# Optimization experiments

Measured on AMD Instinct MI355X. Metric: run time of the kernel, lower is better.

The kernel has to match this reference:

```python
import jax, jax.numpy as jnp
import numpy as np

HEADS = 8
DK = 64   # key_size (defaults to size_per_head)
DV = 64   # size_per_head
RATE = 4
OUT = HEADS * DV  # 512


def extract_seq_patches(x, kernel, rate):
    # x: [b, L, d] -> [b, L, kernel, d]; strided local window gather
    b, L, d = x.shape
    k_size = kernel + (rate - 1) * (kernel - 1)
    p_right = (k_size - 1) // 2
    p_left = k_size - 1 - p_right
    xp = jnp.pad(x, ((0, 0), (p_left, p_right), (0, 0)))
    patches = [xp[:, i:i + L] for i in range(0, k_size, rate)]  # kernel slices
    return jnp.stack(patches, axis=2)


def setup_inputs() -> dict:
    key = jax.random.key(0)
    k1, k2, k3, k4 = jax.random.split(key, 4)
    s = 1.0 / np.sqrt(OUT)
    x = jax.random.normal(k1, (2, 4096, OUT), dtype=jnp.float32)
    Wq = jax.random.normal(k2, (OUT, HEADS * DK), dtype=jnp.float32) * s
    Wk = jax.random.normal(k3, (OUT, HEADS * DK), dtype=jnp.float32) * s
    Wv = jax.random.normal(k4, (OUT, HEADS * DV), dtype=jnp.float32) * s
    return {"x": x, "Wq": Wq, "Wk": Wk, "Wv": Wv}


def reference(x, Wq, Wk, Wv):
    b, L, d = x.shape
    pad = RATE - L % RATE  # torch code always pads (pad=RATE when L % RATE == 0)
    xpad = jnp.pad(x, ((0, 0), (0, pad), (0, 0)))
    nL = L + pad
    n = nL // RATE
    kernel = 2 * RATE - 1  # 1 + 2*neighbors

    qw = xpad @ Wq
    kw = xpad @ Wk
    vw = xpad @ Wv

    kwp = extract_seq_patches(kw, kernel, RATE)  # [b, nL, K, H*dk]
    vwp = extract_seq_patches(vw, kernel, RATE)  # [b, nL, K, H*dv]

    # [b, h, r, n, d]
    qw = qw.reshape(b, n, RATE, HEADS, DK).transpose(0, 3, 2, 1, 4)
    kw = kw.reshape(b, n, RATE, HEADS, DK).transpose(0, 3, 2, 1, 4)
    vw = vw.reshape(b, n, RATE, HEADS, DV).transpose(0, 3, 2, 1, 4)
    # [b, h, r, n, K, d]
    kwp = kwp.reshape(b, n, RATE, kernel, HEADS, DK).transpose(0, 4, 2, 1, 3, 5)
    vwp = vwp.reshape(b, n, RATE, kernel, HEADS, DV).transpose(0, 4, 2, 1, 3, 5)

    scale = 1.0 / np.sqrt(DK)
    a = jnp.einsum('bhrnd,bhrmd->bhrnm', qw, kw) * scale    # strided scores [b,h,r,n,n]
    ap = jnp.einsum('bhrnd,bhrnkd->bhrnk', qw, kwp) * scale  # local scores  [b,h,r,n,K]

    A = jax.nn.softmax(jnp.concatenate([a, ap], axis=-1), axis=-1)
    a, ap = A[..., :n], A[..., n:]

    o = jnp.einsum('bhrnm,bhrmd->bhrnd', a, vw) + jnp.einsum('bhrnk,bhrnkd->bhrnd', ap, vwp)
    o = o.transpose(0, 3, 2, 1, 4).reshape(b, nL, HEADS * DV)
    return o[:, :L]
```

## Files before the change

### kernel.cpp

```cpp
#include <hip/hip_runtime.h>
#include <hip/hip_bf16.h>


#define BATCH 2
#define LSEQ  4096
#define DMODEL 512
#define NH    8
#define DHEAD 64
#define NPAD  1088
#define QSCALE 0.18033688011112042f

typedef __bf16 bf16x8 __attribute__((ext_vector_type(8)));
typedef __attribute__((ext_vector_type(4))) float f32x4;
typedef unsigned short u16;
typedef unsigned int u32;
typedef __attribute__((ext_vector_type(8))) u16 u16x8;
typedef __attribute__((ext_vector_type(4))) u16 u16x4;

__device__ __forceinline__ u16 f2bf(float f) {
    u32 u = __float_as_uint(f);
    u += 0x7fffu + ((u >> 16) & 1u);
    return (u16)(u >> 16);
}

__device__ __forceinline__ u16 cvt_bf(float f) {
    __bf16 t = (__bf16)f;
    return *(const u16*)&t;
}

__device__ __forceinline__ void gload16(const u16* g, u16* l) {
    __builtin_amdgcn_global_load_lds(
        (const __attribute__((address_space(1))) u32*)(const void*)g,
        (__attribute__((address_space(3))) u32*)(void*)l, 16, 0, 0);
}

__global__ __launch_bounds__(256) void prep_kernel(
    const float* __restrict__ x,
    const float* __restrict__ Wq, const float* __restrict__ Wk, const float* __restrict__ Wv,
    u16* __restrict__ xb, u16* __restrict__ Wt)
{
    const int bid = blockIdx.x, tid = threadIdx.x;
    if (bid < 2048) {
        const size_t i0 = (size_t)bid * 2048 + (size_t)tid * 8;
        float4 a = *(const float4*)(x + i0);
        float4 b = *(const float4*)(x + i0 + 4);
        u16x8 o = { f2bf(a.x), f2bf(a.y), f2bf(a.z), f2bf(a.w),
                    f2bf(b.x), f2bf(b.y), f2bf(b.z), f2bf(b.w) };
        *(u16x8*)(xb + i0) = o;
    } else {
        const int wb  = bid - 2048;
        const int mat = wb >> 6;
        const int t   = wb & 63;
        const int k0  = (t >> 3) * 64, c0 = (t & 7) * 64;
        const float* W = (mat == 0) ? Wq : (mat == 1) ? Wk : Wv;
        __shared__ u16 Ws[64][72];
        #pragma unroll
        for (int i = 0; i < 4; ++i) {
            const int chunk = i * 256 + tid;
            const int kr = chunk >> 4, c4 = (chunk & 15) * 4;
            float4 v = *(const float4*)(W + (size_t)(k0 + kr) * DMODEL + c0 + c4);
            u16x4 q = { f2bf(v.x), f2bf(v.y), f2bf(v.z), f2bf(v.w) };
            *(u16x4*)&Ws[kr][c4] = q;
        }
        __syncthreads();
        const int cc = tid >> 2, kq = (tid & 3) * 16;
        alignas(16) u16 tmp[16];
        #pragma unroll
        for (int kk = 0; kk < 16; ++kk) tmp[kk] = Ws[kq + kk][cc];
        u16* dst = Wt + (size_t)(mat * 512 + c0 + cc) * DMODEL + k0 + kq;
        *(u16x8*)dst       = *(const u16x8*)&tmp[0];
        *(u16x8*)(dst + 8) = *(const u16x8*)&tmp[8];
    }
}

__global__ __launch_bounds__(256) void gemm_kernel(
    const u16* __restrict__ xb, const u16* __restrict__ Wt,
    u16* __restrict__ Qb, u16* __restrict__ Kb, u16* __restrict__ Vb)
{
    const int bid = blockIdx.x;
    const int xcd = bid & 7;
    const int j   = bid >> 3;
    const int mt  = xcd * 8 + (j / 12);
    const int nt  = j % 12;
    const int m0 = mt * 128;
    const int n0 = nt * 128;
    const int tid = threadIdx.x;
    const int w = tid >> 6, l = tid & 63, lr = l & 15, lh = l >> 4;
    const int wr = w >> 1, wc = w & 1;

    __shared__ u16 smem[16896];
    u16* As = smem;
    u16* Bs = smem + 8192;

    f32x4 acc[4][4];
    const f32x4 fzero = {0.f, 0.f, 0.f, 0.f};
    #pragma unroll
    for (int mi = 0; mi < 4; ++mi)
        #pragma unroll
        for (int nj = 0; nj < 4; ++nj) acc[mi][nj] = fzero;

    for (int kt = 0; kt < 8; ++kt) {
        const int k0 = kt * 64;
        #pragma unroll
        for (int i = 0; i < 4; ++i) {
            const int cid = i * 256 + tid;
            const int row = cid >> 3, ch = cid & 7;
            const int sch = ch ^ (row & 7);
            u16* dstA = As + (i * 256 + w * 64) * 8;
            u16* dstB = Bs + (i * 256 + w * 64) * 8;
            gload16(xb + (size_t)(m0 + row) * DMODEL + k0 + sch * 8, dstA);
            gload16(Wt + (size_t)(n0 + row) * DMODEL + k0 + sch * 8, dstB);
        }
        __syncthreads();

        #pragma unroll
        for (int kk = 0; kk < 2; ++kk) {
            const int cs = (kk * 4 + lh) ^ (lr & 7);
            bf16x8 af[4], bfr[4];
            #pragma unroll
            for (int mi = 0; mi < 4; ++mi)
                af[mi] = *(const bf16x8*)(As + (wr * 64 + mi * 16 + lr) * 64 + cs * 8);
            #pragma unroll
            for (int nj = 0; nj < 4; ++nj)
                bfr[nj] = *(const bf16x8*)(Bs + (wc * 64 + nj * 16 + lr) * 64 + cs * 8);
            #pragma unroll
            for (int mi = 0; mi < 4; ++mi)
                #pragma unroll
                for (int nj = 0; nj < 4; ++nj)
                    acc[mi][nj] = __builtin_amdgcn_mfma_f32_16x16x32_bf16(af[mi], bfr[nj], acc[mi][nj], 0, 0, 0);
        }
        __syncthreads();
    }

    const int mat = nt >> 2;
    const int hp  = nt & 3;
    if (mat < 2) {
        u16* Ob = (mat == 0) ? Qb : Kb;
        const float osc = (mat == 0) ? QSCALE : 1.0f;
        #pragma unroll
        for (int mi = 0; mi < 4; ++mi) {
            const int gmb = m0 + wr * 64 + mi * 16 + lh * 4;
            const int b = gmb >> 12;
            #pragma unroll
            for (int rr = 0; rr < 4; ++rr) {
                const int t = (gmb + rr) & 4095;
                const int n = t >> 2, r = t & 3;
                #pragma unroll
                for (int nj = 0; nj < 4; ++nj) {
                    const int c  = wc * 64 + nj * 16 + lr;
                    const int h  = hp * 2 + (c >> 6);
                    const int dk = c & 63;
                    const size_t g = ((size_t)(b * NH + h)) * 4 + r;
                    Ob[(g * NPAD + n) * DHEAD + dk] = f2bf(acc[mi][nj][rr] * osc);
                }
            }
        }
    } else {
        #pragma unroll
        for (int mi = 0; mi < 4; ++mi) {
            const int nrel = wr * 16 + mi * 4 + lh;
            #pragma unroll
            for (int nj = 0; nj < 4; ++nj) {
                const int c = wc * 64 + nj * 16 + lr;
                #pragma unroll
                for (int rr = 0; rr < 4; ++rr)
                    smem[c * 132 + rr * 32 + nrel] = f2bf(acc[mi][nj][rr]);
            }
        }
        __syncthreads();
        const int b  = m0 >> 12;
        const int nb = (m0 & 4095) >> 2;
        #pragma unroll
        for (int e = 0; e < 2; ++e) {
            const int chunk = e * 256 + tid;
            const int c = chunk & 127, r = chunk >> 7;
            const int h  = hp * 2 + (c >> 6);
            const int dv = c & 63;
            const size_t g = ((size_t)(b * NH + h)) * 4 + r;
            u16* dst = Vb + (g * DHEAD + dv) * NPAD + nb;
            const u16* src = smem + c * 132 + r * 32;
            alignas(16) u16 tmp[32];
            #pragma unroll
            for (int q8 = 0; q8 < 8; ++q8)
                *(u16x4*)&tmp[q8 * 4] = *(const u16x4*)(src + q8 * 4);
            #pragma unroll
            for (int q16 = 0; q16 < 4; ++q16)
                *(u16x8*)(dst + q16 * 8) = *(const u16x8*)&tmp[q16 * 8];
        }
    }
}

__global__ __launch_bounds__(512) void attn_kernel(
    const u16* __restrict__ Qb, const u16* __restrict__ Kb, const u16* __restrict__ Vb,
    float* __restrict__ out)
{
    const int g  = blockIdx.x;
    const int b  = g >> 5;
    const int h  = (g >> 2) & 7;
    const int r  = g & 3;
    const int q0 = blockIdx.y * 128;
    const int tid = threadIdx.x;
    const int w  = tid >> 6;
    const int l  = tid & 63;
    const int lr = l & 15, lh = l >> 4;

    const u16* Qg  = Qb + (size_t)g * NPAD * DHEAD;
    const u16* Kg  = Kb + (size_t)g * NPAD * DHEAD;
    const u16* Vtg = Vb + (size_t)g * DHEAD * NPAD;

    __shared__ u16 KV[2][2][4096];
    __shared__ u16 Ps[8][16][68];

    const int srow = tid >> 3;
    const int ssch = (tid & 7) ^ (srow & 7);
    const u16* ksrc0 = Kg  + (size_t)srow * DHEAD + ssch * 8;
    const u16* vsrc0 = Vtg + (size_t)srow * NPAD  + ssch * 8;

    bf16x8 qa[2];
    {
        const u16* qrow = Qg + (size_t)(q0 + w * 16 + lr) * DHEAD;
        qa[0] = *(const bf16x8*)(qrow + lh * 8);
        qa[1] = *(const bf16x8*)(qrow + 32 + lh * 8);
    }

    const f32x4 fzero = {0.f, 0.f, 0.f, 0.f};
    f32x4 o[4];
    #pragma unroll
    for (int j = 0; j < 4; ++j) o[j] = fzero;
    float Lpart[4] = {0.f, 0.f, 0.f, 0.f};

    const int qw0 = q0 + w * 16;

    gload16(ksrc0, &KV[0][0][w * 512]);
    gload16(vsrc0, &KV[0][1][w * 512]);

    for (int mt = 0; mt < 16; ++mt) {
        const int cur = mt & 1;
        if (mt < 15) {
            gload16(ksrc0 + (size_t)(mt + 1) * 4096, &KV[cur ^ 1][0][w * 512]);
            gload16(vsrc0 + (mt + 1) * 64,           &KV[cur ^ 1][1][w * 512]);
            asm volatile("s_waitcnt vmcnt(2)" ::: "memory");
        } else {
            asm volatile("s_waitcnt vmcnt(0)" ::: "memory");
        }
        __builtin_amdgcn_s_barrier();

        const u16* Kbuf = KV[cur][0];
        const u16* Vbuf = KV[cur][1];

        f32x4 s[4];
        __builtin_amdgcn_s_setprio(1);
        #pragma unroll
        for (int ni = 0; ni < 4; ++ni) {
            const int rbase = (ni * 16 + lr) * 8;
            const int sl0 = lh ^ (lr & 7), sl1 = (4 + lh) ^ (lr & 7);
            bf16x8 kb0 = *(const bf16x8*)(Kbuf + (rbase + sl0) * 8);
            bf16x8 kb1 = *(const bf16x8*)(Kbuf + (rbase + sl1) * 8);
            f32x4 t = __builtin_amdgcn_mfma_f32_16x16x32_bf16(qa[0], kb0, fzero, 0, 0, 0);
            s[ni] = __builtin_amdgcn_mfma_f32_16x16x32_bf16(qa[1], kb1, t, 0, 0, 0);
        }
        __builtin_amdgcn_s_setprio(0);

        const int m0 = mt * 64;
        const bool special = (m0 + 66 >= qw0) && (m0 <= qw0 + 18);
        if (!special) {
            #pragma unroll
            for (int ni = 0; ni < 4; ++ni) {
                #pragma unroll
                for (int rr = 0; rr < 4; ++rr) {
                    const float p = __builtin_amdgcn_exp2f(s[ni][rr]);
                    Lpart[rr] += p;
                    Ps[w][lh * 4 + rr][ni * 16 + lr] = cvt_bf(p);
                }
            }
        } else {
            #pragma unroll
            for (int ni = 0; ni < 4; ++ni) {
                const int mg = m0 + ni * 16 + lr;
                #pragma unroll
                for (int rr = 0; rr < 4; ++rr) {
                    const int qg = qw0 + lh * 4 + rr;
                    float v = s[ni][rr];
                    const int dd = mg - qg;
                    if (dd >= -3 && dd <= 3) v += 1.0f;
                    const float p = __builtin_amdgcn_exp2f(v);
                    Lpart[rr] += p;
                    Ps[w][lh * 4 + rr][ni * 16 + lr] = cvt_bf(p);
                }
            }
        }

        __builtin_amdgcn_s_setprio(1);
        #pragma unroll
        for (int kk = 0; kk < 2; ++kk) {
            const int slot = (kk * 4 + lh) ^ (lr & 7);
            bf16x8 pa = *(const bf16x8*)&Ps[w][lr][kk * 32 + lh * 8];
            #pragma unroll
            for (int j = 0; j < 4; ++j) {
                bf16x8 vb = *(const bf16x8*)(Vbuf + ((j * 16 + lr) * 8 + slot) * 8);
                o[j] = __builtin_amdgcn_mfma_f32_16x16x32_bf16(pa, vb, o[j], 0, 0, 0);
            }
        }
        __builtin_amdgcn_s_setprio(0);
        __syncthreads();
    }

    #pragma unroll
    for (int rr = 0; rr < 4; ++rr) {
        float s_ = Lpart[rr];
        #pragma unroll
        for (int off = 1; off < 16; off <<= 1)
            s_ += __shfl_xor(s_, off, 16);
        const int qg = qw0 + lh * 4 + rr;
        const int coob = (qg < 3 ? 3 - qg : 0) + (qg > 1021 ? qg - 1021 : 0);
        const float extra = (float)(coob + 1 + (qg >= 1021 ? 1 : 0));
        const float inv = 1.0f / (s_ + extra);
        const int t = qg * 4 + r;
        float* orow = out + ((size_t)b * LSEQ + t) * DMODEL + h * DHEAD;
        #pragma unroll
        for (int j = 0; j < 4; ++j)
            orow[j * 16 + lr] = o[j][rr] * inv;
    }
}

extern "C" void kernel_launch(void* const* d_in, const int* in_sizes, int n_in,
                              void* d_out, int out_size, void* d_ws, size_t ws_size,
                              hipStream_t stream) {
    const float* x  = (const float*)d_in[0];
    const float* Wq = (const float*)d_in[1];
    const float* Wk = (const float*)d_in[2];
    const float* Wv = (const float*)d_in[3];
    float* out = (float*)d_out;

    const size_t SZ = (size_t)BATCH * NH * 4 * NPAD * DHEAD;
    u16* Qb = (u16*)d_ws;
    u16* Kb = Qb + SZ;
    u16* Vb = Kb + SZ;

    u16* xb = (u16*)d_out;
    u16* Wt = xb + (size_t)8192 * 512;

    prep_kernel<<<2240, 256, 0, stream>>>(x, Wq, Wk, Wv, xb, Wt);

    gemm_kernel<<<768, 256, 0, stream>>>(xb, Wt, Qb, Kb, Vb);

    dim3 ga(64, 8);
    attn_kernel<<<ga, 512, 0, stream>>>(Qb, Kb, Vb, out);
}
```

Baseline: 65.43 us.

## Restructure attention kernel around 32x32 MFMA with register-resident probabilities

The attention kernel switches from 16x16x32 to 32x32x16 bf16 MFMAs and computes S transposed (K as A operand), so each wave owns 32 query rows with 4 waves per block instead of 8 waves of 16 rows. Probabilities are packed to bf16 with v_cvt_pk_bf16_f32 and rearranged via cross-half lane shuffles, removing the LDS round trip through the Ps buffer. This is meant to cut LDS traffic and conversion overhead and to improve MFMA efficiency. In exchange it uses more accumulator registers, has fewer waves per block, and writes output with a strided per-row store pattern.

```diff
diff --git a/kernel.cpp b/kernel.cpp
--- a/kernel.cpp
+++ b/kernel.cpp
@@ -12,10 +12,12 @@
 
 typedef __bf16 bf16x8 __attribute__((ext_vector_type(8)));
 typedef __attribute__((ext_vector_type(4))) float f32x4;
+typedef __attribute__((ext_vector_type(16))) float f32x16;
 typedef unsigned short u16;
 typedef unsigned int u32;
 typedef __attribute__((ext_vector_type(8))) u16 u16x8;
 typedef __attribute__((ext_vector_type(4))) u16 u16x4;
+typedef __attribute__((ext_vector_type(4))) u32 u32x4;
 
 __device__ __forceinline__ u16 f2bf(float f) {
     u32 u = __float_as_uint(f);
@@ -23,15 +25,23 @@
     return (u16)(u >> 16);
 }
 
-__device__ __forceinline__ u16 cvt_bf(float f) {
-    __bf16 t = (__bf16)f;
-    return *(const u16*)&t;
+__device__ __forceinline__ u32 cvtpk(float lo, float hi) {
+    u32 d;
+    asm("v_cvt_pk_bf16_f32 %0, %1, %2" : "=v"(d) : "v"(lo), "v"(hi));
+    return d;
 }
 
 __device__ __forceinline__ void gload16(const u16* g, u16* l) {
     __builtin_amdgcn_global_load_lds(
         (const __attribute__((address_space(1))) u32*)(const void*)g,
         (__attribute__((address_space(3))) u32*)(void*)l, 16, 0, 0);
+}
+
+__device__ __forceinline__ f32x16 zero16() {
+    f32x16 v;
+    #pragma unroll
+    for (int i = 0; i < 16; ++i) v[i] = 0.f;
+    return v;
 }
 
 __global__ __launch_bounds__(256) void prep_kernel(
@@ -190,7 +200,7 @@
     }
 }
 
-__global__ __launch_bounds__(512) void attn_kernel(
+__global__ __launch_bounds__(256) void attn_kernel(
     const u16* __restrict__ Qb, const u16* __restrict__ Kb, const u16* __restrict__ Vb,
     float* __restrict__ out)
 {
@@ -202,44 +212,49 @@
     const int tid = threadIdx.x;
     const int w  = tid >> 6;
     const int l  = tid & 63;
-    const int lr = l & 15, lh = l >> 4;
+    const int lr = l & 31;
+    const int hi = l >> 5;
 
     const u16* Qg  = Qb + (size_t)g * NPAD * DHEAD;
     const u16* Kg  = Kb + (size_t)g * NPAD * DHEAD;
     const u16* Vtg = Vb + (size_t)g * DHEAD * NPAD;
 
     __shared__ u16 KV[2][2][4096];
-    __shared__ u16 Ps[8][16][68];
 
     const int srow = tid >> 3;
     const int ssch = (tid & 7) ^ (srow & 7);
     const u16* ksrc0 = Kg  + (size_t)srow * DHEAD + ssch * 8;
     const u16* vsrc0 = Vtg + (size_t)srow * NPAD  + ssch * 8;
 
-    bf16x8 qa[2];
+    bf16x8 qa[4];
     {
-        const u16* qrow = Qg + (size_t)(q0 + w * 16 + lr) * DHEAD;
-        qa[0] = *(const bf16x8*)(qrow + lh * 8);
-        qa[1] = *(const bf16x8*)(qrow + 32 + lh * 8);
-    }
-
-    const f32x4 fzero = {0.f, 0.f, 0.f, 0.f};
-    f32x4 o[4];
-    #pragma unroll
-    for (int j = 0; j < 4; ++j) o[j] = fzero;
-    float Lpart[4] = {0.f, 0.f, 0.f, 0.f};
-
-    const int qw0 = q0 + w * 16;
-
-    gload16(ksrc0, &KV[0][0][w * 512]);
-    gload16(vsrc0, &KV[0][1][w * 512]);
+        const u16* qrow = Qg + (size_t)(q0 + w * 32 + lr) * DHEAD + hi * 8;
+        qa[0] = *(const bf16x8*)(qrow);
+        qa[1] = *(const bf16x8*)(qrow + 16);
+        qa[2] = *(const bf16x8*)(qrow + 32);
+        qa[3] = *(const bf16x8*)(qrow + 48);
+    }
+
+    f32x16 o0 = zero16(), o1 = zero16();
+    float Lown = 0.f;
+    const int qw0 = q0 + w * 32;
+    const int qg  = qw0 + lr;
+
+    gload16(ksrc0,              &KV[0][0][w * 512]);
+    gload16(ksrc0 + 32 * DHEAD, &KV[0][0][2048 + w * 512]);
+    gload16(vsrc0,              &KV[0][1][w * 512]);
+    gload16(vsrc0 + 32 * NPAD,  &KV[0][1][2048 + w * 512]);
 
     for (int mt = 0; mt < 16; ++mt) {
         const int cur = mt & 1;
         if (mt < 15) {
-            gload16(ksrc0 + (size_t)(mt + 1) * 4096, &KV[cur ^ 1][0][w * 512]);
-            gload16(vsrc0 + (mt + 1) * 64,           &KV[cur ^ 1][1][w * 512]);
-            asm volatile("s_waitcnt vmcnt(2)" ::: "memory");
+            const size_t ko = (size_t)(mt + 1) * 64 * DHEAD;
+            const int    vo = (mt + 1) * 64;
+            gload16(ksrc0 + ko,              &KV[cur ^ 1][0][w * 512]);
+            gload16(ksrc0 + ko + 32 * DHEAD, &KV[cur ^ 1][0][2048 + w * 512]);
+            gload16(vsrc0 + vo,              &KV[cur ^ 1][1][w * 512]);
+            gload16(vsrc0 + vo + 32 * NPAD,  &KV[cur ^ 1][1][2048 + w * 512]);
+            asm volatile("s_waitcnt vmcnt(4)" ::: "memory");
         } else {
             asm volatile("s_waitcnt vmcnt(0)" ::: "memory");
         }
@@ -248,78 +263,100 @@
         const u16* Kbuf = KV[cur][0];
         const u16* Vbuf = KV[cur][1];
 
-        f32x4 s[4];
+        f32x16 sA = zero16(), sB = zero16();
         __builtin_amdgcn_s_setprio(1);
         #pragma unroll
-        for (int ni = 0; ni < 4; ++ni) {
-            const int rbase = (ni * 16 + lr) * 8;
-            const int sl0 = lh ^ (lr & 7), sl1 = (4 + lh) ^ (lr & 7);
-            bf16x8 kb0 = *(const bf16x8*)(Kbuf + (rbase + sl0) * 8);
-            bf16x8 kb1 = *(const bf16x8*)(Kbuf + (rbase + sl1) * 8);
-            f32x4 t = __builtin_amdgcn_mfma_f32_16x16x32_bf16(qa[0], kb0, fzero, 0, 0, 0);
-            s[ni] = __builtin_amdgcn_mfma_f32_16x16x32_bf16(qa[1], kb1, t, 0, 0, 0);
+        for (int c = 0; c < 4; ++c) {
+            const int slot = (c * 2 + hi) ^ (lr & 7);
+            bf16x8 kbA = *(const bf16x8*)(Kbuf + (lr * 8 + slot) * 8);
+            bf16x8 kbB = *(const bf16x8*)(Kbuf + ((32 + lr) * 8 + slot) * 8);
+            sA = __builtin_amdgcn_mfma_f32_32x32x16_bf16(kbA, qa[c], sA, 0, 0, 0);
+            sB = __builtin_amdgcn_mfma_f32_32x32x16_bf16(kbB, qa[c], sB, 0, 0, 0);
         }
         __builtin_amdgcn_s_setprio(0);
 
         const int m0 = mt * 64;
-        const bool special = (m0 + 66 >= qw0) && (m0 <= qw0 + 18);
+        const bool special = (m0 + 66 >= qw0) && (m0 <= qw0 + 34);
         if (!special) {
             #pragma unroll
-            for (int ni = 0; ni < 4; ++ni) {
-                #pragma unroll
-                for (int rr = 0; rr < 4; ++rr) {
-                    const float p = __builtin_amdgcn_exp2f(s[ni][rr]);
-                    Lpart[rr] += p;
-                    Ps[w][lh * 4 + rr][ni * 16 + lr] = cvt_bf(p);
-                }
+            for (int reg = 0; reg < 16; ++reg) {
+                sA[reg] = __builtin_amdgcn_exp2f(sA[reg]);
+                sB[reg] = __builtin_amdgcn_exp2f(sB[reg]);
+                Lown += sA[reg] + sB[reg];
             }
         } else {
             #pragma unroll
-            for (int ni = 0; ni < 4; ++ni) {
-                const int mg = m0 + ni * 16 + lr;
-                #pragma unroll
-                for (int rr = 0; rr < 4; ++rr) {
-                    const int qg = qw0 + lh * 4 + rr;
-                    float v = s[ni][rr];
-                    const int dd = mg - qg;
+            for (int reg = 0; reg < 16; ++reg) {
+                const int krel = (reg & 3) + 8 * (reg >> 2) + 4 * hi;
+                {
+                    const int dd = m0 + krel - qg;
+                    float v = sA[reg];
                     if (dd >= -3 && dd <= 3) v += 1.0f;
-                    const float p = __builtin_amdgcn_exp2f(v);
-                    Lpart[rr] += p;
-                    Ps[w][lh * 4 + rr][ni * 16 + lr] = cvt_bf(p);
+                    sA[reg] = __builtin_amdgcn_exp2f(v);
                 }
+                {
+                    const int dd = m0 + 32 + krel - qg;
+                    float v = sB[reg];
+                    if (dd >= -3 && dd <= 3) v += 1.0f;
+                    sB[reg] = __builtin_amdgcn_exp2f(v);
+                }
+                Lown += sA[reg] + sB[reg];
             }
         }
 
+        u32 pkA[8], pkB[8];
+        #pragma unroll
+        for (int r2 = 0; r2 < 8; ++r2) {
+            pkA[r2] = cvtpk(sA[2 * r2], sA[2 * r2 + 1]);
+            pkB[r2] = cvtpk(sB[2 * r2], sB[2 * r2 + 1]);
+        }
+
         __builtin_amdgcn_s_setprio(1);
         #pragma unroll
-        for (int kk = 0; kk < 2; ++kk) {
-            const int slot = (kk * 4 + lh) ^ (lr & 7);
-            bf16x8 pa = *(const bf16x8*)&Ps[w][lr][kk * 32 + lh * 8];
-            #pragma unroll
-            for (int j = 0; j < 4; ++j) {
-                bf16x8 vb = *(const bf16x8*)(Vbuf + ((j * 16 + lr) * 8 + slot) * 8);
-                o[j] = __builtin_amdgcn_mfma_f32_16x16x32_bf16(pa, vb, o[j], 0, 0, 0);
-            }
+        for (int c = 0; c < 4; ++c) {
+            const int c1 = c & 1;
+            u32 p0, p1, p2, p3;
+            if (c < 2) { p0 = pkA[4*c1]; p1 = pkA[4*c1+1]; p2 = pkA[4*c1+2]; p3 = pkA[4*c1+3]; }
+            else       { p0 = pkB[4*c1]; p1 = pkB[4*c1+1]; p2 = pkB[4*c1+2]; p3 = pkB[4*c1+3]; }
+            const u32 own0  = hi ? p2 : p0;
+            const u32 own1  = hi ? p3 : p1;
+            const u32 send0 = hi ? p0 : p2;
+            const u32 send1 = hi ? p1 : p3;
+            const u32 recv0 = (u32)__shfl_xor((int)send0, 32);
+            const u32 recv1 = (u32)__shfl_xor((int)send1, 32);
+            u32x4 paw;
+            paw.x = hi ? recv0 : own0;
+            paw.y = hi ? recv1 : own1;
+            paw.z = hi ? own0  : recv0;
+            paw.w = hi ? own1  : recv1;
+            const bf16x8 pa = __builtin_bit_cast(bf16x8, paw);
+
+            const int slot = (c * 2 + hi) ^ (lr & 7);
+            bf16x8 vb0 = *(const bf16x8*)(Vbuf + (lr * 8 + slot) * 8);
+            bf16x8 vb1 = *(const bf16x8*)(Vbuf + ((32 + lr) * 8 + slot) * 8);
+            o0 = __builtin_amdgcn_mfma_f32_32x32x16_bf16(pa, vb0, o0, 0, 0, 0);
+            o1 = __builtin_amdgcn_mfma_f32_32x32x16_bf16(pa, vb1, o1, 0, 0, 0);
         }
         __builtin_amdgcn_s_setprio(0);
         __syncthreads();
     }
 
+    const float Ltot = Lown + __shfl_xor(Lown, 32);
+    const int coob = (qg < 3 ? 3 - qg : 0) + (qg > 1021 ? qg - 1021 : 0);
+    const float inv = 1.0f / (Ltot + (float)(coob + 1 + (qg >= 1021 ? 1 : 0)));
+
+    float iv[16];
     #pragma unroll
-    for (int rr = 0; rr < 4; ++rr) {
-        float s_ = Lpart[rr];
-        #pragma unroll
-        for (int off = 1; off < 16; off <<= 1)
-            s_ += __shfl_xor(s_, off, 16);
-        const int qg = qw0 + lh * 4 + rr;
-        const int coob = (qg < 3 ? 3 - qg : 0) + (qg > 1021 ? qg - 1021 : 0);
-        const float extra = (float)(coob + 1 + (qg >= 1021 ? 1 : 0));
-        const float inv = 1.0f / (s_ + extra);
-        const int t = qg * 4 + r;
+    for (int reg = 0; reg < 16; ++reg)
+        iv[reg] = __shfl(inv, (reg & 3) + 8 * (reg >> 2) + 4 * hi);
+
+    #pragma unroll
+    for (int reg = 0; reg < 16; ++reg) {
+        const int qrel = (reg & 3) + 8 * (reg >> 2) + 4 * hi;
+        const int t = (q0 + w * 32 + qrel) * 4 + r;
         float* orow = out + ((size_t)b * LSEQ + t) * DMODEL + h * DHEAD;
-        #pragma unroll
-        for (int j = 0; j < 4; ++j)
-            orow[j * 16 + lr] = o[j][rr] * inv;
+        orow[lr]      = o0[reg] * iv[reg];
+        orow[32 + lr] = o1[reg] * iv[reg];
     }
 }
 
@@ -345,5 +382,5 @@
     gemm_kernel<<<768, 256, 0, stream>>>(xb, Wt, Qb, Kb, Vb);
 
     dim3 ga(64, 8);
-    attn_kernel<<<ga, 512, 0, stream>>>(Qb, Kb, Vb, out);
-}
+    attn_kernel<<<ga, 256, 0, stream>>>(Qb, Kb, Vb, out);
+}
```

Measured after the change: 67.68 us. +3.4%, slower.

## Keep softmax probabilities in registers via transposed MFMA and triple-buffer K/V

Applied to the files above, without the earlier changes.

Swaps the MFMA operand order so score tiles come out transposed, packs probabilities to bf16 with v_cvt_pk_bf16_f32, and rearranges them across lanes with shuffles into the PV operand. This removes the per-wave LDS staging buffer for P. K/V loads go from double to triple buffering, which drops the trailing __syncthreads per iteration. Output stores become float4 per lane, and launch bounds request 4 waves per SIMD. In exchange it adds cross-lane shuffles and uses more LDS for the third K/V buffer.

```diff
diff --git a/kernel.cpp b/kernel.cpp
--- a/kernel.cpp
+++ b/kernel.cpp
@@ -16,6 +16,7 @@
 typedef unsigned int u32;
 typedef __attribute__((ext_vector_type(8))) u16 u16x8;
 typedef __attribute__((ext_vector_type(4))) u16 u16x4;
+typedef __attribute__((ext_vector_type(4))) u32 u32x4;
 
 __device__ __forceinline__ u16 f2bf(float f) {
     u32 u = __float_as_uint(f);
@@ -23,9 +24,10 @@
     return (u16)(u >> 16);
 }
 
-__device__ __forceinline__ u16 cvt_bf(float f) {
-    __bf16 t = (__bf16)f;
-    return *(const u16*)&t;
+__device__ __forceinline__ u32 cvtpk(float lo, float hi) {
+    u32 d;
+    asm("v_cvt_pk_bf16_f32 %0, %1, %2" : "=v"(d) : "v"(lo), "v"(hi));
+    return d;
 }
 
 __device__ __forceinline__ void gload16(const u16* g, u16* l) {
@@ -190,7 +192,7 @@
     }
 }
 
-__global__ __launch_bounds__(512) void attn_kernel(
+__global__ __launch_bounds__(512, 4) void attn_kernel(
     const u16* __restrict__ Qb, const u16* __restrict__ Kb, const u16* __restrict__ Vb,
     float* __restrict__ out)
 {
@@ -208,8 +210,7 @@
     const u16* Kg  = Kb + (size_t)g * NPAD * DHEAD;
     const u16* Vtg = Vb + (size_t)g * DHEAD * NPAD;
 
-    __shared__ u16 KV[2][2][4096];
-    __shared__ u16 Ps[8][16][68];
+    __shared__ u16 KV[3][2][4096];
 
     const int srow = tid >> 3;
     const int ssch = (tid & 7) ^ (srow & 7);
@@ -227,26 +228,28 @@
     f32x4 o[4];
     #pragma unroll
     for (int j = 0; j < 4; ++j) o[j] = fzero;
-    float Lpart[4] = {0.f, 0.f, 0.f, 0.f};
+    float Lown = 0.f;
 
     const int qw0 = q0 + w * 16;
-
-    gload16(ksrc0, &KV[0][0][w * 512]);
-    gload16(vsrc0, &KV[0][1][w * 512]);
+    const int qg  = qw0 + lr;
+
+    gload16(ksrc0,              &KV[0][0][w * 512]);
+    gload16(vsrc0,              &KV[0][1][w * 512]);
+    gload16(ksrc0 + 64 * DHEAD, &KV[1][0][w * 512]);
+    gload16(vsrc0 + 64,         &KV[1][1][w * 512]);
 
     for (int mt = 0; mt < 16; ++mt) {
-        const int cur = mt & 1;
-        if (mt < 15) {
-            gload16(ksrc0 + (size_t)(mt + 1) * 4096, &KV[cur ^ 1][0][w * 512]);
-            gload16(vsrc0 + (mt + 1) * 64,           &KV[cur ^ 1][1][w * 512]);
-            asm volatile("s_waitcnt vmcnt(2)" ::: "memory");
-        } else {
-            asm volatile("s_waitcnt vmcnt(0)" ::: "memory");
-        }
+        if (mt < 15) asm volatile("s_waitcnt vmcnt(2)" ::: "memory");
+        else         asm volatile("s_waitcnt vmcnt(0)" ::: "memory");
         __builtin_amdgcn_s_barrier();
-
-        const u16* Kbuf = KV[cur][0];
-        const u16* Vbuf = KV[cur][1];
+        if (mt < 14) {
+            const int nb = (mt + 2) % 3;
+            gload16(ksrc0 + (size_t)(mt + 2) * 64 * DHEAD, &KV[nb][0][w * 512]);
+            gload16(vsrc0 + (mt + 2) * 64,                 &KV[nb][1][w * 512]);
+        }
+
+        const u16* Kbuf = KV[mt % 3][0];
+        const u16* Vbuf = KV[mt % 3][1];
 
         f32x4 s[4];
         __builtin_amdgcn_s_setprio(1);
@@ -256,8 +259,8 @@
             const int sl0 = lh ^ (lr & 7), sl1 = (4 + lh) ^ (lr & 7);
             bf16x8 kb0 = *(const bf16x8*)(Kbuf + (rbase + sl0) * 8);
             bf16x8 kb1 = *(const bf16x8*)(Kbuf + (rbase + sl1) * 8);
-            f32x4 t = __builtin_amdgcn_mfma_f32_16x16x32_bf16(qa[0], kb0, fzero, 0, 0, 0);
-            s[ni] = __builtin_amdgcn_mfma_f32_16x16x32_bf16(qa[1], kb1, t, 0, 0, 0);
+            f32x4 t = __builtin_amdgcn_mfma_f32_16x16x32_bf16(kb0, qa[0], fzero, 0, 0, 0);
+            s[ni] = __builtin_amdgcn_mfma_f32_16x16x32_bf16(kb1, qa[1], t, 0, 0, 0);
         }
         __builtin_amdgcn_s_setprio(0);
 
@@ -265,61 +268,69 @@
         const bool special = (m0 + 66 >= qw0) && (m0 <= qw0 + 18);
         if (!special) {
             #pragma unroll
-            for (int ni = 0; ni < 4; ++ni) {
+            for (int ni = 0; ni < 4; ++ni)
                 #pragma unroll
                 for (int rr = 0; rr < 4; ++rr) {
                     const float p = __builtin_amdgcn_exp2f(s[ni][rr]);
-                    Lpart[rr] += p;
-                    Ps[w][lh * 4 + rr][ni * 16 + lr] = cvt_bf(p);
+                    s[ni][rr] = p;
+                    Lown += p;
                 }
-            }
         } else {
             #pragma unroll
-            for (int ni = 0; ni < 4; ++ni) {
-                const int mg = m0 + ni * 16 + lr;
+            for (int ni = 0; ni < 4; ++ni)
                 #pragma unroll
                 for (int rr = 0; rr < 4; ++rr) {
-                    const int qg = qw0 + lh * 4 + rr;
+                    const int dd = m0 + ni * 16 + lh * 4 + rr - qg;
                     float v = s[ni][rr];
-                    const int dd = mg - qg;
                     if (dd >= -3 && dd <= 3) v += 1.0f;
                     const float p = __builtin_amdgcn_exp2f(v);
-                    Lpart[rr] += p;
-                    Ps[w][lh * 4 + rr][ni * 16 + lr] = cvt_bf(p);
+                    s[ni][rr] = p;
+                    Lown += p;
                 }
+        }
+
+        u32 pk[4][2];
+        #pragma unroll
+        for (int ni = 0; ni < 4; ++ni) {
+            pk[ni][0] = cvtpk(s[ni][0], s[ni][1]);
+            pk[ni][1] = cvtpk(s[ni][2], s[ni][3]);
+        }
+
+        __builtin_amdgcn_s_setprio(1);
+        #pragma unroll
+        for (int kk = 0; kk < 2; ++kk) {
+            u32 wd[4];
+            #pragma unroll
+            for (int j2 = 0; j2 < 4; ++j2) {
+                const int srcl = ((lh & 1) * 2 + (j2 >> 1)) * 16 + lr;
+                const u32 a0 = (u32)__shfl((int)pk[2 * kk + 0][j2 & 1], srcl);
+                const u32 a1 = (u32)__shfl((int)pk[2 * kk + 1][j2 & 1], srcl);
+                wd[j2] = (lh >= 2) ? a1 : a0;
             }
-        }
-
-        __builtin_amdgcn_s_setprio(1);
-        #pragma unroll
-        for (int kk = 0; kk < 2; ++kk) {
+            u32x4 paw = { wd[0], wd[1], wd[2], wd[3] };
+            const bf16x8 pb = __builtin_bit_cast(bf16x8, paw);
+
             const int slot = (kk * 4 + lh) ^ (lr & 7);
-            bf16x8 pa = *(const bf16x8*)&Ps[w][lr][kk * 32 + lh * 8];
-            #pragma unroll
-            for (int j = 0; j < 4; ++j) {
-                bf16x8 vb = *(const bf16x8*)(Vbuf + ((j * 16 + lr) * 8 + slot) * 8);
-                o[j] = __builtin_amdgcn_mfma_f32_16x16x32_bf16(pa, vb, o[j], 0, 0, 0);
+            #pragma unroll
+            for (int dj = 0; dj < 4; ++dj) {
+                bf16x8 vb = *(const bf16x8*)(Vbuf + ((dj * 16 + lr) * 8 + slot) * 8);
+                o[dj] = __builtin_amdgcn_mfma_f32_16x16x32_bf16(vb, pb, o[dj], 0, 0, 0);
             }
         }
         __builtin_amdgcn_s_setprio(0);
-        __syncthreads();
-    }
-
+    }
+
+    Lown += __shfl_xor(Lown, 16);
+    Lown += __shfl_xor(Lown, 32);
+    const int coob = (qg < 3 ? 3 - qg : 0) + (qg > 1021 ? qg - 1021 : 0);
+    const float inv = 1.0f / (Lown + (float)(coob + 1 + (qg >= 1021 ? 1 : 0)));
+
+    const int t = qg * 4 + r;
+    float* orow = out + ((size_t)b * LSEQ + t) * DMODEL + h * DHEAD;
     #pragma unroll
-    for (int rr = 0; rr < 4; ++rr) {
-        float s_ = Lpart[rr];
-        #pragma unroll
-        for (int off = 1; off < 16; off <<= 1)
-            s_ += __shfl_xor(s_, off, 16);
-        const int qg = qw0 + lh * 4 + rr;
-        const int coob = (qg < 3 ? 3 - qg : 0) + (qg > 1021 ? qg - 1021 : 0);
-        const float extra = (float)(coob + 1 + (qg >= 1021 ? 1 : 0));
-        const float inv = 1.0f / (s_ + extra);
-        const int t = qg * 4 + r;
-        float* orow = out + ((size_t)b * LSEQ + t) * DMODEL + h * DHEAD;
-        #pragma unroll
-        for (int j = 0; j < 4; ++j)
-            orow[j * 16 + lr] = o[j][rr] * inv;
+    for (int dj = 0; dj < 4; ++dj) {
+        float4 v = { o[dj][0] * inv, o[dj][1] * inv, o[dj][2] * inv, o[dj][3] * inv };
+        *(float4*)(orow + dj * 16 + lh * 4) = v;
     }
 }
 
```

Measured after the change: 69.00 us. 1.05x slower.

## Use 1024-thread attention blocks with two-tile steps and quad-buffered K/V

Applied to the files above, without the earlier changes.

The attention kernel now launches 1024 threads per block, each block covering 256 queries, so each K/V tile loaded into shared memory is reused by twice as many waves. The loop processes two 64-key tiles per iteration from a four-slot ring buffer, which halves the number of barrier iterations and drops the trailing __syncthreads. Each group of 8 waves loads one of the two upcoming tiles. The costs are fewer blocks in the grid (256 instead of 512), more shared memory per block, higher register pressure from the doubled score tiles, and reliance on the ring-buffer slot reuse being safe without the trailing sync.

```diff
diff --git a/kernel.cpp b/kernel.cpp
--- a/kernel.cpp
+++ b/kernel.cpp
@@ -190,7 +190,7 @@
     }
 }
 
-__global__ __launch_bounds__(512) void attn_kernel(
+__global__ __launch_bounds__(1024, 4) void attn_kernel(
     const u16* __restrict__ Qb, const u16* __restrict__ Kb, const u16* __restrict__ Vb,
     float* __restrict__ out)
 {
@@ -198,7 +198,7 @@
     const int b  = g >> 5;
     const int h  = (g >> 2) & 7;
     const int r  = g & 3;
-    const int q0 = blockIdx.y * 128;
+    const int q0 = blockIdx.y * 256;
     const int tid = threadIdx.x;
     const int w  = tid >> 6;
     const int l  = tid & 63;
@@ -208,13 +208,16 @@
     const u16* Kg  = Kb + (size_t)g * NPAD * DHEAD;
     const u16* Vtg = Vb + (size_t)g * DHEAD * NPAD;
 
-    __shared__ u16 KV[2][2][4096];
-    __shared__ u16 Ps[8][16][68];
-
-    const int srow = tid >> 3;
-    const int ssch = (tid & 7) ^ (srow & 7);
+    __shared__ u16 KV[4][2][4096];
+    __shared__ u16 PsA[16][16][68];
+    __shared__ u16 PsB[16][16][68];
+
+    const int stile = w >> 3;
+    const int srow  = (tid >> 3) & 63;
+    const int ssch  = (tid & 7) ^ (srow & 7);
     const u16* ksrc0 = Kg  + (size_t)srow * DHEAD + ssch * 8;
     const u16* vsrc0 = Vtg + (size_t)srow * NPAD  + ssch * 8;
+    const int sbase = (w & 7) * 512;
 
     bf16x8 qa[2];
     {
@@ -231,61 +234,92 @@
 
     const int qw0 = q0 + w * 16;
 
-    gload16(ksrc0, &KV[0][0][w * 512]);
-    gload16(vsrc0, &KV[0][1][w * 512]);
-
-    for (int mt = 0; mt < 16; ++mt) {
-        const int cur = mt & 1;
-        if (mt < 15) {
-            gload16(ksrc0 + (size_t)(mt + 1) * 4096, &KV[cur ^ 1][0][w * 512]);
-            gload16(vsrc0 + (mt + 1) * 64,           &KV[cur ^ 1][1][w * 512]);
-            asm volatile("s_waitcnt vmcnt(2)" ::: "memory");
-        } else {
-            asm volatile("s_waitcnt vmcnt(0)" ::: "memory");
-        }
+    gload16(ksrc0 + (size_t)stile * 64 * DHEAD, &KV[stile][0][sbase]);
+    gload16(vsrc0 + stile * 64,                 &KV[stile][1][sbase]);
+
+    for (int it = 0; it < 8; ++it) {
+        asm volatile("s_waitcnt vmcnt(0)" ::: "memory");
         __builtin_amdgcn_s_barrier();
-
-        const u16* Kbuf = KV[cur][0];
-        const u16* Vbuf = KV[cur][1];
-
-        f32x4 s[4];
+        if (it < 7) {
+            const int t = 2 * it + 2 + stile;
+            gload16(ksrc0 + (size_t)t * 64 * DHEAD, &KV[t & 3][0][sbase]);
+            gload16(vsrc0 + t * 64,                 &KV[t & 3][1][sbase]);
+        }
+
+        const u16* KbufA = KV[(2 * it) & 3][0];
+        const u16* VbufA = KV[(2 * it) & 3][1];
+        const u16* KbufB = KV[(2 * it + 1) & 3][0];
+        const u16* VbufB = KV[(2 * it + 1) & 3][1];
+
+        f32x4 sA[4], sB[4];
         __builtin_amdgcn_s_setprio(1);
         #pragma unroll
         for (int ni = 0; ni < 4; ++ni) {
             const int rbase = (ni * 16 + lr) * 8;
             const int sl0 = lh ^ (lr & 7), sl1 = (4 + lh) ^ (lr & 7);
-            bf16x8 kb0 = *(const bf16x8*)(Kbuf + (rbase + sl0) * 8);
-            bf16x8 kb1 = *(const bf16x8*)(Kbuf + (rbase + sl1) * 8);
-            f32x4 t = __builtin_amdgcn_mfma_f32_16x16x32_bf16(qa[0], kb0, fzero, 0, 0, 0);
-            s[ni] = __builtin_amdgcn_mfma_f32_16x16x32_bf16(qa[1], kb1, t, 0, 0, 0);
+            bf16x8 ka0 = *(const bf16x8*)(KbufA + (rbase + sl0) * 8);
+            bf16x8 ka1 = *(const bf16x8*)(KbufA + (rbase + sl1) * 8);
+            f32x4 tA = __builtin_amdgcn_mfma_f32_16x16x32_bf16(qa[0], ka0, fzero, 0, 0, 0);
+            sA[ni] = __builtin_amdgcn_mfma_f32_16x16x32_bf16(qa[1], ka1, tA, 0, 0, 0);
+            bf16x8 kb0 = *(const bf16x8*)(KbufB + (rbase + sl0) * 8);
+            bf16x8 kb1 = *(const bf16x8*)(KbufB + (rbase + sl1) * 8);
+            f32x4 tB = __builtin_amdgcn_mfma_f32_16x16x32_bf16(qa[0], kb0, fzero, 0, 0, 0);
+            sB[ni] = __builtin_amdgcn_mfma_f32_16x16x32_bf16(qa[1], kb1, tB, 0, 0, 0);
         }
         __builtin_amdgcn_s_setprio(0);
 
-        const int m0 = mt * 64;
-        const bool special = (m0 + 66 >= qw0) && (m0 <= qw0 + 18);
-        if (!special) {
+        const int m0A = it * 128;
+        const bool spA = (m0A + 66 >= qw0) && (m0A <= qw0 + 18);
+        if (!spA) {
+            #pragma unroll
+            for (int ni = 0; ni < 4; ++ni)
+                #pragma unroll
+                for (int rr = 0; rr < 4; ++rr) {
+                    const float p = __builtin_amdgcn_exp2f(sA[ni][rr]);
+                    Lpart[rr] += p;
+                    PsA[w][lh * 4 + rr][ni * 16 + lr] = cvt_bf(p);
+                }
+        } else {
             #pragma unroll
             for (int ni = 0; ni < 4; ++ni) {
-                #pragma unroll
-                for (int rr = 0; rr < 4; ++rr) {
-                    const float p = __builtin_amdgcn_exp2f(s[ni][rr]);
-                    Lpart[rr] += p;
-                    Ps[w][lh * 4 + rr][ni * 16 + lr] = cvt_bf(p);
-                }
-            }
-        } else {
-            #pragma unroll
-            for (int ni = 0; ni < 4; ++ni) {
-                const int mg = m0 + ni * 16 + lr;
+                const int mg = m0A + ni * 16 + lr;
                 #pragma unroll
                 for (int rr = 0; rr < 4; ++rr) {
                     const int qg = qw0 + lh * 4 + rr;
-                    float v = s[ni][rr];
+                    float v = sA[ni][rr];
                     const int dd = mg - qg;
                     if (dd >= -3 && dd <= 3) v += 1.0f;
                     const float p = __builtin_amdgcn_exp2f(v);
                     Lpart[rr] += p;
-                    Ps[w][lh * 4 + rr][ni * 16 + lr] = cvt_bf(p);
+                    PsA[w][lh * 4 + rr][ni * 16 + lr] = cvt_bf(p);
+                }
+            }
+        }
+
+        const int m0B = it * 128 + 64;
+        const bool spB = (m0B + 66 >= qw0) && (m0B <= qw0 + 18);
+        if (!spB) {
+            #pragma unroll
+            for (int ni = 0; ni < 4; ++ni)
+                #pragma unroll
+                for (int rr = 0; rr < 4; ++rr) {
+                    const float p = __builtin_amdgcn_exp2f(sB[ni][rr]);
+                    Lpart[rr] += p;
+                    PsB[w][lh * 4 + rr][ni * 16 + lr] = cvt_bf(p);
+                }
+        } else {
+            #pragma unroll
+            for (int ni = 0; ni < 4; ++ni) {
+                const int mg = m0B + ni * 16 + lr;
+                #pragma unroll
+                for (int rr = 0; rr < 4; ++rr) {
+                    const int qg = qw0 + lh * 4 + rr;
+                    float v = sB[ni][rr];
+                    const int dd = mg - qg;
+                    if (dd >= -3 && dd <= 3) v += 1.0f;
+                    const float p = __builtin_amdgcn_exp2f(v);
+                    Lpart[rr] += p;
+                    PsB[w][lh * 4 + rr][ni * 16 + lr] = cvt_bf(p);
                 }
             }
         }
@@ -294,15 +328,17 @@
         #pragma unroll
         for (int kk = 0; kk < 2; ++kk) {
             const int slot = (kk * 4 + lh) ^ (lr & 7);
-            bf16x8 pa = *(const bf16x8*)&Ps[w][lr][kk * 32 + lh * 8];
+            bf16x8 paA = *(const bf16x8*)&PsA[w][lr][kk * 32 + lh * 8];
+            bf16x8 paB = *(const bf16x8*)&PsB[w][lr][kk * 32 + lh * 8];
             #pragma unroll
             for (int j = 0; j < 4; ++j) {
-                bf16x8 vb = *(const bf16x8*)(Vbuf + ((j * 16 + lr) * 8 + slot) * 8);
-                o[j] = __builtin_amdgcn_mfma_f32_16x16x32_bf16(pa, vb, o[j], 0, 0, 0);
+                bf16x8 vbA = *(const bf16x8*)(VbufA + ((j * 16 + lr) * 8 + slot) * 8);
+                o[j] = __builtin_amdgcn_mfma_f32_16x16x32_bf16(paA, vbA, o[j], 0, 0, 0);
+                bf16x8 vbB = *(const bf16x8*)(VbufB + ((j * 16 + lr) * 8 + slot) * 8);
+                o[j] = __builtin_amdgcn_mfma_f32_16x16x32_bf16(paB, vbB, o[j], 0, 0, 0);
             }
         }
         __builtin_amdgcn_s_setprio(0);
-        __syncthreads();
     }
 
     #pragma unroll
@@ -344,6 +380,6 @@
 
     gemm_kernel<<<768, 256, 0, stream>>>(xb, Wt, Qb, Kb, Vb);
 
-    dim3 ga(64, 8);
-    attn_kernel<<<ga, 512, 0, stream>>>(Qb, Kb, Vb, out);
-}
+    dim3 ga(64, 4);
+    attn_kernel<<<ga, 1024, 0, stream>>>(Qb, Kb, Vb, out);
+}
```

Result: no change. 65.51 us (+0.1%).
